# Kernel optimization log

Measured on AMD Instinct MI355X. Metric: run time of the kernel, lower is better.

Reference implementation:

```python
import jax, jax.numpy as jnp
import numpy as np
from jax import lax

B, M = 16384, 128
NUM_LAYERS, OW, OH = 22, 11, 11
MAX_VEC = np.array([9.0, 1.0, 1.0, 10.0, 3.0, 254.0, 1.0, 1.0, 235.0, 8.0, 9.0, 250.0,
                    29.0, 1.0, 1.0, 8.0, 1.0, 1.0, 6.0, 3.0, 1.0, 2.0], dtype=np.float32)


def setup_inputs() -> dict:
    key = jax.random.key(0)
    ks = jax.random.split(key, 20)
    s = 0.05
    return {
        "observations": jax.random.randint(ks[0], (B, M, 3), 0, 255, dtype=jnp.int32),
        "cnn1_w": jax.random.normal(ks[1], (64, 22, 5, 5), jnp.float32) * s,
        "cnn1_b": jnp.zeros((64,), jnp.float32),
        "cnn2_w": jax.random.normal(ks[2], (64, 64, 3, 3), jnp.float32) * s,
        "cnn2_b": jnp.zeros((64,), jnp.float32),
        "fc1_w": jax.random.normal(ks[3], (128, 64), jnp.float32) * s,
        "fc1_b": jnp.zeros((128,), jnp.float32),
        "enc_w": jax.random.normal(ks[4], (128, 128), jnp.float32) * s,
        "enc_b": jnp.zeros((128,), jnp.float32),
        "critic1_w": jax.random.normal(ks[5], (1024, 128), jnp.float32) * s,
        "critic1_b": jnp.zeros((1024,), jnp.float32),
        "value_w": jax.random.normal(ks[6], (1, 1024), jnp.float32) * s,
        "value_b": jnp.zeros((1,), jnp.float32),
        "actor1_w": jax.random.normal(ks[7], (512, 128), jnp.float32) * s,
        "actor1_b": jnp.zeros((512,), jnp.float32),
        "action_emb": jax.random.normal(ks[8], (100, 16), jnp.float32) * s,
        "head0_w": jax.random.normal(ks[9], (9, 528), jnp.float32) * s,
        "head0_b": jnp.zeros((9,), jnp.float32),
        "head1_w": jax.random.normal(ks[10], (10, 528), jnp.float32) * s,
        "head1_b": jnp.zeros((10,), jnp.float32),
    }


def _encode_scatter(observations):
    # zero-out any byte equal to 255 (matches torch in-place masking)
    tok = jnp.where(observations == 255, 0, observations)  # [B, M, 3]
    coords = tok[..., 0].astype(jnp.uint8)
    x = ((coords >> 4) & 15).astype(jnp.int32)
    y = (coords & 15).astype(jnp.int32)
    atr = tok[..., 1].astype(jnp.int32)
    val = tok[..., 2].astype(jnp.float32)
    b, m = atr.shape
    valid = (x < OW) & (y < OH) & (atr < NUM_LAYERS)
    b_idx = jnp.broadcast_to(jnp.arange(b, dtype=jnp.int32)[:, None], (b, m))
    b_idx = jnp.where(valid, b_idx, b)  # route invalid tokens out of bounds -> dropped
    box = jnp.zeros((b, NUM_LAYERS, OW, OH), jnp.float32)
    box = box.at[b_idx, atr, x, y].set(val, mode="drop")
    return box


def _forward(observations, cnn1_w, cnn1_b, cnn2_w, cnn2_b, fc1_w, fc1_b, enc_w, enc_b,
             critic1_w, critic1_b, value_w, value_b, actor1_w, actor1_b, action_emb,
             head0_w, head0_b, head1_w, head1_b):
    box = _encode_scatter(observations)
    x = box / jnp.asarray(MAX_VEC)[None, :, None, None]
    dn = ("NCHW", "OIHW", "NCHW")
    x = lax.conv_general_dilated(x, cnn1_w, (3, 3), "VALID", dimension_numbers=dn) + cnn1_b[None, :, None, None]
    x = lax.conv_general_dilated(x, cnn2_w, (1, 1), "VALID", dimension_numbers=dn) + cnn2_b[None, :, None, None]
    x = x.reshape(x.shape[0], -1)                 # [B, 64]
    x = x @ fc1_w.T + fc1_b                       # [B, 128]
    hidden = x @ enc_w.T + enc_b                  # [B, 128]
    critic = jnp.tanh(hidden @ critic1_w.T + critic1_b)
    value = critic @ value_w.T + value_b          # [B, 1]
    actor = hidden @ actor1_w.T + actor1_b        # [B, 512]
    emb = jnp.broadcast_to(action_emb.mean(axis=0)[None, :], (actor.shape[0], action_emb.shape[1]))
    comb = jnp.concatenate([actor, emb], axis=-1)  # [B, 528]
    logits = jnp.concatenate([comb @ head0_w.T + head0_b, comb @ head1_w.T + head1_b], axis=-1)
    return logits, value


def reference(observations, cnn1_w, cnn1_b, cnn2_w, cnn2_b, fc1_w, fc1_b, enc_w, enc_b,
              critic1_w, critic1_b, value_w, value_b, actor1_w, actor1_b, action_emb,
              head0_w, head0_b, head1_w, head1_b):
    return _forward(observations, cnn1_w, cnn1_b, cnn2_w, cnn2_b, fc1_w, fc1_b, enc_w, enc_b,
                    critic1_w, critic1_b, value_w, value_b, actor1_w, actor1_b, action_emb,
                    head0_w, head0_b, head1_w, head1_b)
```

## Files before the change

kernel.cpp:

```cpp
#include <hip/hip_runtime.h>
#include <math.h>

#define NB 16384
#define NTOK 128
#define NKEY 2662
#define NLOG 19
#define TB 32

typedef __attribute__((ext_vector_type(8))) short short8;
typedef __attribute__((ext_vector_type(4))) float floatx4;

__device__ __constant__ float c_maxv[22] = {
    9.f, 1.f, 1.f, 10.f, 3.f, 254.f, 1.f, 1.f, 235.f, 8.f, 9.f, 250.f,
    29.f, 1.f, 1.f, 8.f, 1.f, 1.f, 6.f, 3.f, 1.f, 2.f};

__device__ __forceinline__ unsigned short f2bf(float f) {
    unsigned u = __float_as_uint(f);
    return (unsigned short)((u + 0x7FFFu + ((u >> 16) & 1u)) >> 16);
}
__device__ __forceinline__ float tanh_fast(float x) {
    float e = __builtin_amdgcn_exp2f(x * 2.885390082f);
    return 1.f - 2.f * __builtin_amdgcn_rcpf(e + 1.f);
}

__global__ __launch_bounds__(256) void k_pre1(
    const float* __restrict__ w1, const float* __restrict__ b1,
    const float* __restrict__ w2, const float* __restrict__ b2,
    const float* __restrict__ fc1w, const float* __restrict__ encw,
    const float* __restrict__ h0w, const float* __restrict__ h1w,
    const float* __restrict__ a1w, const float* __restrict__ aemb,
    const float* __restrict__ c1w,
    float* __restrict__ G, float* __restrict__ E,
    float* __restrict__ h2b, float* __restrict__ emb,
    float* __restrict__ Wlog, unsigned short* __restrict__ c1wb)
{
    __shared__ float s_w2[72 * 65];
    const int bid = blockIdx.x, t = threadIdx.x;
    if (bid < 666) {
        const int v = t & 63;
        const int key_u = __builtin_amdgcn_readfirstlane(bid * 4 + (t >> 6));
        const int key_c = (key_u < NKEY) ? key_u : (NKEY - 1);
        const int c = key_c / 121, rem = key_c % 121, X = rem / 11, Y = rem % 11;

        const int vg0 = t / 72, rg0 = t - vg0 * 72;
        const int base0 = vg0 * 576 + rg0;

        float rw[18];
        {
            int rg = rg0, base = base0;
            #pragma unroll
            for (int r = 0; r < 18; ++r) {
                rw[r] = w2[base];
                rg += 40; base += 1768;
                if (rg >= 72) { rg -= 72; base += 504; }
            }
        }
        float acc = 0.f;
        for (int s = 0; s < 8; ++s) {
            __syncthreads();
            {
                int rg = rg0, vg = vg0;
                #pragma unroll
                for (int r = 0; r < 18; ++r) {
                    s_w2[rg * 65 + vg] = rw[r];
                    rg += 40; vg += 3;
                    if (rg >= 72) { rg -= 72; vg += 1; }
                }
            }
            __syncthreads();
            if (s < 7) {
                int rg = rg0, base = base0 + (s + 1) * 72;
                #pragma unroll
                for (int r = 0; r < 18; ++r) {
                    rw[r] = w2[base];
                    rg += 40; base += 1768;
                    if (rg >= 72) { rg -= 72; base += 504; }
                }
            }
            const int u0 = s * 8;
            #pragma unroll
            for (int ur = 0; ur < 8; ++ur) {
                const int w1base = (u0 + ur) * 550 + c * 25;
                #pragma unroll
                for (int i = 0; i < 3; ++i) {
                    int xi = X - 3 * i;
                    if (xi < 0 || xi > 4) continue;
                    #pragma unroll
                    for (int j = 0; j < 3; ++j) {
                        int yj = Y - 3 * j;
                        if (yj < 0 || yj > 4) continue;
                        acc += s_w2[(ur * 9 + i * 3 + j) * 65 + v] *
                               w1[w1base + xi * 5 + yj];
                    }
                }
            }
        }
        if (key_u < NKEY) G[key_u * 64 + v] = acc;
    } else if (bid < 698) {
        int m = (bid - 666) * 256 + t;
        int h = __builtin_amdgcn_readfirstlane(m >> 6) & 127;
        int v = t & 63;
        float acc = 0.f;
        #pragma unroll 8
        for (int p = 0; p < 128; ++p)
            acc += encw[h * 128 + p] * fc1w[p * 64 + v];
        E[h * 64 + v] = acc;
    } else if (bid == 698) {
        int o = t >> 2, q = t & 3;
        const float* wp = w2 + (o * 64 + q * 16) * 9;
        float s = 0.f;
        #pragma unroll
        for (int ui = 0; ui < 16; ++ui) {
            float ws = 0.f;
            #pragma unroll
            for (int k = 0; k < 9; ++k) ws += wp[ui * 9 + k];
            s += b1[q * 16 + ui] * ws;
        }
        s += __shfl_xor(s, 1, 64);
        s += __shfl_xor(s, 2, 64);
        if (q == 0) h2b[o] = s + b2[o];
    } else if (bid == 699) {
        if (t < 64) {
            int e = t & 15, rq = t >> 4;
            float s = 0.f;
            #pragma unroll
            for (int rr = 0; rr < 25; ++rr) s += aemb[(rq * 25 + rr) * 16 + e];
            s += __shfl_xor(s, 16, 64);
            s += __shfl_xor(s, 32, 64);
            if (t < 16) emb[e] = s * 0.01f;
        }
    } else if (bid < 710) {
        int n = (bid - 700) * 256 + t;
        if (n < NLOG * 128) {
            int o = __builtin_amdgcn_readfirstlane(n >> 7);
            int h = n & 127;
            const float* hw = (o < 9) ? (h0w + o * 528) : (h1w + (o - 9) * 528);
            float acc = 0.f;
            #pragma unroll 8
            for (int a = 0; a < 512; ++a)
                acc += hw[a] * a1w[a * 128 + h];
            Wlog[n] = acc;
        }
    } else {
        int n = (bid - 710) * 256 + t;
        c1wb[n] = f2bf(c1w[n]);
    }
}

__global__ __launch_bounds__(256) void k_pre2(
    const float* __restrict__ G, const float* __restrict__ E,
    const float* __restrict__ h2b, const float* __restrict__ emb,
    const float* __restrict__ fc1w, const float* __restrict__ fc1b,
    const float* __restrict__ encw, const float* __restrict__ encb,
    const float* __restrict__ a1b,
    const float* __restrict__ h0w, const float* __restrict__ h0b,
    const float* __restrict__ h1w, const float* __restrict__ h1b,
    float* __restrict__ Weff, float* __restrict__ beff, float* __restrict__ blog)
{
    __shared__ float s_h2[64];
    __shared__ float s_t[128];
    const int bid = blockIdx.x, t = threadIdx.x;
    if (bid < 1331) {
        int n = bid * 256 + t;
        int key = __builtin_amdgcn_readfirstlane(n >> 7);
        int h = n & 127;
        const float4* E4 = (const float4*)E;
        const float4* G4 = (const float4*)(G + key * 64);
        float acc = 0.f;
        #pragma unroll
        for (int vq = 0; vq < 16; ++vq) {
            float4 e = E4[h * 16 + vq];
            float4 g = G4[vq];
            acc += e.x * g.x + e.y * g.y + e.z * g.z + e.w * g.w;
        }
        Weff[n] = acc / c_maxv[key / 121];
    } else {
        if (t < 64) s_h2[t] = h2b[t];
        __syncthreads();
        if (t < 128) {
            const float4* f4 = (const float4*)(fc1w + t * 64);
            float s = fc1b[t];
            #pragma unroll
            for (int vq = 0; vq < 16; ++vq) {
                float4 w = f4[vq];
                s += w.x * s_h2[vq * 4]     + w.y * s_h2[vq * 4 + 1] +
                     w.z * s_h2[vq * 4 + 2] + w.w * s_h2[vq * 4 + 3];
            }
            s_t[t] = s;
        } else {
            int tp = t - 128;
            int os = tp >> 3, ai = tp & 7;
            #pragma unroll
            for (int rep = 0; rep < 2; ++rep) {
                int o = os + rep * 16;
                int oc = (o < NLOG) ? o : (NLOG - 1);
                const float* hw = (oc < 9) ? (h0w + oc * 528)
                                           : (h1w + (oc - 9) * 528);
                float s = 0.f;
                for (int a = ai; a < 528; a += 8) {
                    float m = (a < 512) ? a1b[a] : emb[a - 512];
                    s += hw[a] * m;
                }
                s += __shfl_xor(s, 1, 64);
                s += __shfl_xor(s, 2, 64);
                s += __shfl_xor(s, 4, 64);
                if (ai == 0 && o < NLOG)
                    blog[o] = s + ((o < 9) ? h0b[o] : h1b[o - 9]);
            }
        }
        __syncthreads();
        if (t < 128) {
            const float4* e4 = (const float4*)(encw + t * 128);
            float s = encb[t];
            #pragma unroll
            for (int pq = 0; pq < 32; ++pq) {
                float4 w = e4[pq];
                s += w.x * s_t[pq * 4]     + w.y * s_t[pq * 4 + 1] +
                     w.z * s_t[pq * 4 + 2] + w.w * s_t[pq * 4 + 3];
            }
            beff[t] = s;
        }
    }
}

__global__ __launch_bounds__(512, 4) void k_main(
    const int* __restrict__ obs,
    const float* __restrict__ Weff, const float* __restrict__ beff,
    const unsigned short* __restrict__ c1wb, const float* __restrict__ c1b,
    const float* __restrict__ vw, const float* __restrict__ vb,
    const float* __restrict__ Wlog, const float* __restrict__ blog,
    float* __restrict__ out)
{
    __shared__ int            s_lst[TB * 32];
    __shared__ float          s_hidden[TB * 128];
    __shared__ unsigned short s_hb[TB * 136];
    __shared__ int            s_cnt[TB];
    __shared__ float          s_val[8 * 32];

    const int tid = threadIdx.x, bid = blockIdx.x;
    const int b0 = bid * TB;

    if (tid < TB) s_cnt[tid] = 0;
    __syncthreads();

    {
        const int gtok0 = b0 * NTOK;
        #pragma unroll
        for (int k = 0; k < TB * NTOK / (512 * 4); ++k) {
            int g = tid + 512 * k;
            const int4* p = (const int4*)(obs + (size_t)(gtok0 + 4 * g) * 3);
            int4 A = p[0], Bv = p[1], Cv = p[2];
            int d[12] = {A.x, A.y, A.z, A.w, Bv.x, Bv.y, Bv.z, Bv.w,
                         Cv.x, Cv.y, Cv.z, Cv.w};
            #pragma unroll
            for (int s = 0; s < 4; ++s) {
                int o0 = d[3 * s], o1 = d[3 * s + 1], o2 = d[3 * s + 2];
                o0 = (o0 == 255) ? 0 : o0;
                o1 = (o1 == 255) ? 0 : o1;
                o2 = (o2 == 255) ? 0 : o2;
                int x = (o0 >> 4) & 15, y = o0 & 15;
                if (x < 11 && y < 11 && o1 < 22) {
                    int tt = 4 * g + s;
                    int bb = tt >> 7, m = tt & 127;
                    int pos = atomicAdd(&s_cnt[bb], 1);
                    if (pos < 32)
                        s_lst[bb * 32 + pos] =
                            (m << 20) | (o2 << 12) | (o1 * 121 + x * 11 + y);
                }
            }
        }
    }
    __syncthreads();

    {
        int bb = tid >> 4, e0 = tid & 15;
        int n = s_cnt[bb]; if (n > 32) n = 32;
        #pragma unroll
        for (int r = 0; r < 2; ++r) {
            int e = e0 + 16 * r;
            if (e < n) {
                int p = s_lst[bb * 32 + e];
                bool dead = false;
                for (int i = 0; i < n; ++i) {
                    int q = s_lst[bb * 32 + i];
                    dead |= (((q ^ p) & 0xFFF) == 0) && (q > p);
                }
                if (dead) s_lst[bb * 32 + e] = p & ~0x000FF000;
            }
        }
    }
    __syncthreads();

    {
        int h = tid & 127, bg = tid >> 7;
        float be = beff[h];
        #pragma unroll
        for (int it = 0; it < 4; ++it) {
            int bbA = bg + it * 8, bbB = bbA + 4;
            int nA = s_cnt[bbA]; if (nA > 32) nA = 32;
            int nB = s_cnt[bbB]; if (nB > 32) nB = 32;
            int nm = (nA > nB) ? nA : nB;
            float aA = be, aB = be;
            for (int i = 0; i < nm; ++i) {
                if (i < nA) {
                    int p = s_lst[bbA * 32 + i];
                    aA += (float)((p >> 12) & 0xFF) * Weff[(p & 0xFFF) * 128 + h];
                }
                if (i < nB) {
                    int p = s_lst[bbB * 32 + i];
                    aB += (float)((p >> 12) & 0xFF) * Weff[(p & 0xFFF) * 128 + h];
                }
            }
            s_hidden[bbA * 128 + h] = aA; s_hb[bbA * 136 + h] = f2bf(aA);
            s_hidden[bbB * 128 + h] = aB; s_hb[bbB * 136 + h] = f2bf(aB);
        }
    }
    __syncthreads();

    {
        const int lane = tid & 63, w = tid >> 6;
        const int lm = lane & 15, quad = lane >> 4;
        short8 af0[4], af1[4];
        #pragma unroll
        for (int kk = 0; kk < 4; ++kk) {
            af0[kk] = *(const short8*)&s_hb[lm * 136 + kk * 32 + quad * 8];
            af1[kk] = *(const short8*)&s_hb[(16 + lm) * 136 + kk * 32 + quad * 8];
        }
        float vp0[4] = {0.f, 0.f, 0.f, 0.f}, vp1[4] = {0.f, 0.f, 0.f, 0.f};
        for (int nt = 0; nt < 8; ++nt) {
            int j = w * 128 + nt * 16 + lm;
            const short8* cp = (const short8*)&c1wb[j * 128];
            floatx4 a0 = {0.f, 0.f, 0.f, 0.f}, a1 = {0.f, 0.f, 0.f, 0.f};
            #pragma unroll
            for (int kk = 0; kk < 4; ++kk) {
                short8 bf = cp[kk * 4 + quad];
                a0 = __builtin_amdgcn_mfma_f32_16x16x32_bf16(af0[kk], bf, a0, 0, 0, 0);
                a1 = __builtin_amdgcn_mfma_f32_16x16x32_bf16(af1[kk], bf, a1, 0, 0, 0);
            }
            float bj = c1b[j], wj = vw[j];
            #pragma unroll
            for (int r = 0; r < 4; ++r) {
                vp0[r] += tanh_fast(a0[r] + bj) * wj;
                vp1[r] += tanh_fast(a1[r] + bj) * wj;
            }
        }
        #pragma unroll
        for (int off = 1; off <= 8; off <<= 1) {
            #pragma unroll
            for (int r = 0; r < 4; ++r) {
                vp0[r] += __shfl_xor(vp0[r], off, 64);
                vp1[r] += __shfl_xor(vp1[r], off, 64);
            }
        }
        if (lm == 0) {
            #pragma unroll
            for (int r = 0; r < 4; ++r) {
                s_val[w * 32 + quad * 4 + r]      = vp0[r];
                s_val[w * 32 + 16 + quad * 4 + r] = vp1[r];
            }
        }
    }
    __syncthreads();
    if (tid < TB) {
        float v = 0.f;
        #pragma unroll
        for (int w = 0; w < 8; ++w) v += s_val[w * 32 + tid];
        out[NB * NLOG + b0 + tid] = v + vb[0];
    }

    {
        const float4* s_h4 = (const float4*)s_hidden;
        const float4* wl4  = (const float4*)Wlog;
        int bl = tid >> 4, oo = tid & 15;
        #pragma unroll
        for (int rep = 0; rep < 2; ++rep) {
            int o = oo + rep * 16;
            if (o < NLOG) {
                float acc = blog[o];
                #pragma unroll
                for (int hq = 0; hq < 32; ++hq) {
                    float4 hv = s_h4[bl * 32 + hq];
                    float4 wl = wl4[o * 32 + hq];
                    acc += wl.x * hv.x + wl.y * hv.y + wl.z * hv.z + wl.w * hv.w;
                }
                out[(b0 + bl) * NLOG + o] = acc;
            }
        }
    }
}

extern "C" void kernel_launch(void* const* d_in, const int* in_sizes, int n_in,
                              void* d_out, int out_size, void* d_ws, size_t ws_size,
                              hipStream_t stream)
{
    const int*   obs  = (const int*)  d_in[0];
    const float* w1   = (const float*)d_in[1];
    const float* b1   = (const float*)d_in[2];
    const float* w2   = (const float*)d_in[3];
    const float* b2   = (const float*)d_in[4];
    const float* fc1w = (const float*)d_in[5];
    const float* fc1b = (const float*)d_in[6];
    const float* encw = (const float*)d_in[7];
    const float* encb = (const float*)d_in[8];
    const float* c1w  = (const float*)d_in[9];
    const float* c1b  = (const float*)d_in[10];
    const float* vw   = (const float*)d_in[11];
    const float* vb   = (const float*)d_in[12];
    const float* a1w  = (const float*)d_in[13];
    const float* a1b  = (const float*)d_in[14];
    const float* aemb = (const float*)d_in[15];
    const float* h0w  = (const float*)d_in[16];
    const float* h0b  = (const float*)d_in[17];
    const float* h1w  = (const float*)d_in[18];
    const float* h1b  = (const float*)d_in[19];

    float* W    = (float*)d_ws;
    float* G    = W;
    float* E    = W + 170368;
    float* h2b  = W + 178560;
    float* emb  = W + 178624;
    float* Weff = W + 178640;
    float* beff = W + 519376;
    float* Wlog = W + 519504;
    float* blog = W + 521936;
    unsigned short* c1wb = (unsigned short*)(W + 524288);

    hipLaunchKernelGGL(k_pre1, dim3(1222), dim3(256), 0, stream,
                       w1, b1, w2, b2, fc1w, encw, h0w, h1w, a1w, aemb, c1w,
                       G, E, h2b, emb, Wlog, c1wb);
    hipLaunchKernelGGL(k_pre2, dim3(1332), dim3(256), 0, stream,
                       G, E, h2b, emb, fc1w, fc1b, encw, encb, a1b,
                       h0w, h0b, h1w, h1b, Weff, beff, blog);
    hipLaunchKernelGGL(k_main, dim3(NB / TB), dim3(512), 0, stream,
                       obs, Weff, beff, c1wb, c1b, vw, vb, Wlog, blog,
                       (float*)d_out);
}
```

Measured before the change: 214.7 us.

## Drop Weff precompute; gather 64-wide G and apply E per tile in main kernel

Removes the second preprocessing kernel that built the 2662x128 effective weight table. The main kernel now gathers from the smaller 64-wide G table into shared memory, then applies the transposed E matrix (staged in LDS) with a small per-tile matmul. The small bias and logit-bias computations are folded into one block of the single preprocessing kernel, and the bf16 weight conversion is vectorised. This saves a launch and halves the gather width, but adds 32KB of LDS plus an extra matmul stage in k_main, which may lower occupancy.

```diff
diff --git a/kernel.cpp b/kernel.cpp
--- a/kernel.cpp
+++ b/kernel.cpp
@@ -23,61 +23,40 @@
     return 1.f - 2.f * __builtin_amdgcn_rcpf(e + 1.f);
 }
 
-__global__ __launch_bounds__(256) void k_pre1(
+__global__ __launch_bounds__(256) void k_pre(
     const float* __restrict__ w1, const float* __restrict__ b1,
     const float* __restrict__ w2, const float* __restrict__ b2,
-    const float* __restrict__ fc1w, const float* __restrict__ encw,
-    const float* __restrict__ h0w, const float* __restrict__ h1w,
-    const float* __restrict__ a1w, const float* __restrict__ aemb,
+    const float* __restrict__ fc1w, const float* __restrict__ fc1b,
+    const float* __restrict__ encw, const float* __restrict__ encb,
+    const float* __restrict__ a1w, const float* __restrict__ a1b,
+    const float* __restrict__ aemb,
+    const float* __restrict__ h0w, const float* __restrict__ h0b,
+    const float* __restrict__ h1w, const float* __restrict__ h1b,
     const float* __restrict__ c1w,
     float* __restrict__ G, float* __restrict__ E,
-    float* __restrict__ h2b, float* __restrict__ emb,
-    float* __restrict__ Wlog, unsigned short* __restrict__ c1wb)
+    float* __restrict__ beff, float* __restrict__ Wlog,
+    float* __restrict__ blog, unsigned short* __restrict__ c1wb)
 {
     __shared__ float s_w2[72 * 65];
+    __shared__ float s_h2[64];
+    __shared__ float s_t[128];
+    __shared__ float s_emb[16];
     const int bid = blockIdx.x, t = threadIdx.x;
     if (bid < 666) {
         const int v = t & 63;
         const int key_u = __builtin_amdgcn_readfirstlane(bid * 4 + (t >> 6));
         const int key_c = (key_u < NKEY) ? key_u : (NKEY - 1);
         const int c = key_c / 121, rem = key_c % 121, X = rem / 11, Y = rem % 11;
-
-        const int vg0 = t / 72, rg0 = t - vg0 * 72;
-        const int base0 = vg0 * 576 + rg0;
-
-        float rw[18];
-        {
-            int rg = rg0, base = base0;
+        float acc = 0.f;
+        for (int u0 = 0; u0 < 64; u0 += 8) {
+            __syncthreads();
             #pragma unroll
             for (int r = 0; r < 18; ++r) {
-                rw[r] = w2[base];
-                rg += 40; base += 1768;
-                if (rg >= 72) { rg -= 72; base += 504; }
-            }
-        }
-        float acc = 0.f;
-        for (int s = 0; s < 8; ++s) {
+                int g = t + 256 * r;
+                int vg = g / 72, rg = g % 72;
+                s_w2[rg * 65 + vg] = w2[vg * 576 + u0 * 9 + rg];
+            }
             __syncthreads();
-            {
-                int rg = rg0, vg = vg0;
-                #pragma unroll
-                for (int r = 0; r < 18; ++r) {
-                    s_w2[rg * 65 + vg] = rw[r];
-                    rg += 40; vg += 3;
-                    if (rg >= 72) { rg -= 72; vg += 1; }
-                }
-            }
-            __syncthreads();
-            if (s < 7) {
-                int rg = rg0, base = base0 + (s + 1) * 72;
-                #pragma unroll
-                for (int r = 0; r < 18; ++r) {
-                    rw[r] = w2[base];
-                    rg += 40; base += 1768;
-                    if (rg >= 72) { rg -= 72; base += 504; }
-                }
-            }
-            const int u0 = s * 8;
             #pragma unroll
             for (int ur = 0; ur < 8; ++ur) {
                 const int w1base = (u0 + ur) * 550 + c * 25;
@@ -95,7 +74,7 @@
                 }
             }
         }
-        if (key_u < NKEY) G[key_u * 64 + v] = acc;
+        if (key_u < NKEY) G[key_u * 64 + v] = acc / c_maxv[c];
     } else if (bid < 698) {
         int m = (bid - 666) * 256 + t;
         int h = __builtin_amdgcn_readfirstlane(m >> 6) & 127;
@@ -104,33 +83,78 @@
         #pragma unroll 8
         for (int p = 0; p < 128; ++p)
             acc += encw[h * 128 + p] * fc1w[p * 64 + v];
-        E[h * 64 + v] = acc;
+        E[v * 128 + h] = acc;
     } else if (bid == 698) {
-        int o = t >> 2, q = t & 3;
-        const float* wp = w2 + (o * 64 + q * 16) * 9;
-        float s = 0.f;
-        #pragma unroll
-        for (int ui = 0; ui < 16; ++ui) {
-            float ws = 0.f;
-            #pragma unroll
-            for (int k = 0; k < 9; ++k) ws += wp[ui * 9 + k];
-            s += b1[q * 16 + ui] * ws;
-        }
-        s += __shfl_xor(s, 1, 64);
-        s += __shfl_xor(s, 2, 64);
-        if (q == 0) h2b[o] = s + b2[o];
-    } else if (bid == 699) {
-        if (t < 64) {
-            int e = t & 15, rq = t >> 4;
+        {
+            int o = t >> 2, q = t & 3;
+            const float* wp = w2 + (o * 64 + q * 16) * 9;
+            float s = 0.f;
+            #pragma unroll
+            for (int ui = 0; ui < 16; ++ui) {
+                float ws = 0.f;
+                #pragma unroll
+                for (int k = 0; k < 9; ++k) ws += wp[ui * 9 + k];
+                s += b1[q * 16 + ui] * ws;
+            }
+            s += __shfl_xor(s, 1, 64);
+            s += __shfl_xor(s, 2, 64);
+            if (q == 0) s_h2[o] = s + b2[o];
+        }
+        __syncthreads();
+        if (t < 128) {
+            const float4* f4 = (const float4*)(fc1w + t * 64);
+            float s = fc1b[t];
+            #pragma unroll
+            for (int vq = 0; vq < 16; ++vq) {
+                float4 w = f4[vq];
+                s += w.x * s_h2[vq * 4]     + w.y * s_h2[vq * 4 + 1] +
+                     w.z * s_h2[vq * 4 + 2] + w.w * s_h2[vq * 4 + 3];
+            }
+            s_t[t] = s;
+        } else if (t < 192) {
+            int lane = t & 63;
+            int e = lane & 15, rq = lane >> 4;
             float s = 0.f;
             #pragma unroll
             for (int rr = 0; rr < 25; ++rr) s += aemb[(rq * 25 + rr) * 16 + e];
             s += __shfl_xor(s, 16, 64);
             s += __shfl_xor(s, 32, 64);
-            if (t < 16) emb[e] = s * 0.01f;
-        }
-    } else if (bid < 710) {
-        int n = (bid - 700) * 256 + t;
+            if (lane < 16) s_emb[e] = s * 0.01f;
+        }
+        __syncthreads();
+        if (t < 128) {
+            const float4* e4 = (const float4*)(encw + t * 128);
+            float s = encb[t];
+            #pragma unroll
+            for (int pq = 0; pq < 32; ++pq) {
+                float4 w = e4[pq];
+                s += w.x * s_t[pq * 4]     + w.y * s_t[pq * 4 + 1] +
+                     w.z * s_t[pq * 4 + 2] + w.w * s_t[pq * 4 + 3];
+            }
+            beff[t] = s;
+        } else {
+            int tp = t - 128;
+            int os = tp >> 3, ai = tp & 7;
+            #pragma unroll
+            for (int rep = 0; rep < 2; ++rep) {
+                int o = os + rep * 16;
+                int oc = (o < NLOG) ? o : (NLOG - 1);
+                const float* hw = (oc < 9) ? (h0w + oc * 528)
+                                           : (h1w + (oc - 9) * 528);
+                float s = 0.f;
+                for (int a = ai; a < 528; a += 8) {
+                    float m = (a < 512) ? a1b[a] : s_emb[a - 512];
+                    s += hw[a] * m;
+                }
+                s += __shfl_xor(s, 1, 64);
+                s += __shfl_xor(s, 2, 64);
+                s += __shfl_xor(s, 4, 64);
+                if (ai == 0 && o < NLOG)
+                    blog[o] = s + ((o < 9) ? h0b[o] : h1b[o - 9]);
+            }
+        }
+    } else if (bid < 709) {
+        int n = (bid - 699) * 256 + t;
         if (n < NLOG * 128) {
             int o = __builtin_amdgcn_readfirstlane(n >> 7);
             int h = n & 127;
@@ -142,90 +166,22 @@
             Wlog[n] = acc;
         }
     } else {
-        int n = (bid - 710) * 256 + t;
-        c1wb[n] = f2bf(c1w[n]);
-    }
-}
-
-__global__ __launch_bounds__(256) void k_pre2(
-    const float* __restrict__ G, const float* __restrict__ E,
-    const float* __restrict__ h2b, const float* __restrict__ emb,
-    const float* __restrict__ fc1w, const float* __restrict__ fc1b,
-    const float* __restrict__ encw, const float* __restrict__ encb,
-    const float* __restrict__ a1b,
-    const float* __restrict__ h0w, const float* __restrict__ h0b,
-    const float* __restrict__ h1w, const float* __restrict__ h1b,
-    float* __restrict__ Weff, float* __restrict__ beff, float* __restrict__ blog)
-{
-    __shared__ float s_h2[64];
-    __shared__ float s_t[128];
-    const int bid = blockIdx.x, t = threadIdx.x;
-    if (bid < 1331) {
-        int n = bid * 256 + t;
-        int key = __builtin_amdgcn_readfirstlane(n >> 7);
-        int h = n & 127;
-        const float4* E4 = (const float4*)E;
-        const float4* G4 = (const float4*)(G + key * 64);
-        float acc = 0.f;
-        #pragma unroll
-        for (int vq = 0; vq < 16; ++vq) {
-            float4 e = E4[h * 16 + vq];
-            float4 g = G4[vq];
-            acc += e.x * g.x + e.y * g.y + e.z * g.z + e.w * g.w;
-        }
-        Weff[n] = acc / c_maxv[key / 121];
-    } else {
-        if (t < 64) s_h2[t] = h2b[t];
-        __syncthreads();
-        if (t < 128) {
-            const float4* f4 = (const float4*)(fc1w + t * 64);
-            float s = fc1b[t];
-            #pragma unroll
-            for (int vq = 0; vq < 16; ++vq) {
-                float4 w = f4[vq];
-                s += w.x * s_h2[vq * 4]     + w.y * s_h2[vq * 4 + 1] +
-                     w.z * s_h2[vq * 4 + 2] + w.w * s_h2[vq * 4 + 3];
-            }
-            s_t[t] = s;
-        } else {
-            int tp = t - 128;
-            int os = tp >> 3, ai = tp & 7;
-            #pragma unroll
-            for (int rep = 0; rep < 2; ++rep) {
-                int o = os + rep * 16;
-                int oc = (o < NLOG) ? o : (NLOG - 1);
-                const float* hw = (oc < 9) ? (h0w + oc * 528)
-                                           : (h1w + (oc - 9) * 528);
-                float s = 0.f;
-                for (int a = ai; a < 528; a += 8) {
-                    float m = (a < 512) ? a1b[a] : emb[a - 512];
-                    s += hw[a] * m;
-                }
-                s += __shfl_xor(s, 1, 64);
-                s += __shfl_xor(s, 2, 64);
-                s += __shfl_xor(s, 4, 64);
-                if (ai == 0 && o < NLOG)
-                    blog[o] = s + ((o < 9) ? h0b[o] : h1b[o - 9]);
-            }
-        }
-        __syncthreads();
-        if (t < 128) {
-            const float4* e4 = (const float4*)(encw + t * 128);
-            float s = encb[t];
-            #pragma unroll
-            for (int pq = 0; pq < 32; ++pq) {
-                float4 w = e4[pq];
-                s += w.x * s_t[pq * 4]     + w.y * s_t[pq * 4 + 1] +
-                     w.z * s_t[pq * 4 + 2] + w.w * s_t[pq * 4 + 3];
-            }
-            beff[t] = s;
-        }
+        int n = ((bid - 709) * 256 + t) * 8;
+        float4 a = *(const float4*)(c1w + n);
+        float4 b4 = *(const float4*)(c1w + n + 4);
+        short8 r;
+        r[0] = (short)f2bf(a.x);  r[1] = (short)f2bf(a.y);
+        r[2] = (short)f2bf(a.z);  r[3] = (short)f2bf(a.w);
+        r[4] = (short)f2bf(b4.x); r[5] = (short)f2bf(b4.y);
+        r[6] = (short)f2bf(b4.z); r[7] = (short)f2bf(b4.w);
+        *(short8*)(c1wb + n) = r;
     }
 }
 
 __global__ __launch_bounds__(512, 4) void k_main(
     const int* __restrict__ obs,
-    const float* __restrict__ Weff, const float* __restrict__ beff,
+    const float* __restrict__ G, const float* __restrict__ E,
+    const float* __restrict__ beff,
     const unsigned short* __restrict__ c1wb, const float* __restrict__ c1b,
     const float* __restrict__ vw, const float* __restrict__ vb,
     const float* __restrict__ Wlog, const float* __restrict__ blog,
@@ -234,11 +190,17 @@
     __shared__ int            s_lst[TB * 32];
     __shared__ float          s_hidden[TB * 128];
     __shared__ unsigned short s_hb[TB * 136];
+    __shared__ float          s_x[TB * 64];
+    __shared__ float          s_E[8192];
     __shared__ int            s_cnt[TB];
     __shared__ float          s_val[8 * 32];
 
     const int tid = threadIdx.x, bid = blockIdx.x;
     const int b0 = bid * TB;
+
+    const float4* E4g = (const float4*)E;
+    float4 e0 = E4g[tid], e1 = E4g[tid + 512],
+           e2 = E4g[tid + 1024], e3 = E4g[tid + 1536];
 
     if (tid < TB) s_cnt[tid] = 0;
     __syncthreads();
@@ -269,15 +231,18 @@
                 }
             }
         }
-    }
-    __syncthreads();
-
-    {
-        int bb = tid >> 4, e0 = tid & 15;
+        float4* sE4 = (float4*)s_E;
+        sE4[tid] = e0; sE4[tid + 512] = e1;
+        sE4[tid + 1024] = e2; sE4[tid + 1536] = e3;
+    }
+    __syncthreads();
+
+    {
+        int bb = tid >> 4, e0i = tid & 15;
         int n = s_cnt[bb]; if (n > 32) n = 32;
         #pragma unroll
         for (int r = 0; r < 2; ++r) {
-            int e = e0 + 16 * r;
+            int e = e0i + 16 * r;
             if (e < n) {
                 int p = s_lst[bb * 32 + e];
                 bool dead = false;
@@ -292,27 +257,54 @@
     __syncthreads();
 
     {
-        int h = tid & 127, bg = tid >> 7;
-        float be = beff[h];
-        #pragma unroll
-        for (int it = 0; it < 4; ++it) {
-            int bbA = bg + it * 8, bbB = bbA + 4;
+        int w = tid >> 6, lane = tid & 63;
+        #pragma unroll
+        for (int jp = 0; jp < 2; ++jp) {
+            int bbA = w * 4 + jp * 2, bbB = bbA + 1;
             int nA = s_cnt[bbA]; if (nA > 32) nA = 32;
             int nB = s_cnt[bbB]; if (nB > 32) nB = 32;
             int nm = (nA > nB) ? nA : nB;
-            float aA = be, aB = be;
+            float aA = 0.f, aB = 0.f;
             for (int i = 0; i < nm; ++i) {
                 if (i < nA) {
                     int p = s_lst[bbA * 32 + i];
-                    aA += (float)((p >> 12) & 0xFF) * Weff[(p & 0xFFF) * 128 + h];
+                    aA += (float)((p >> 12) & 0xFF) * G[(p & 0xFFF) * 64 + lane];
                 }
                 if (i < nB) {
                     int p = s_lst[bbB * 32 + i];
-                    aB += (float)((p >> 12) & 0xFF) * Weff[(p & 0xFFF) * 128 + h];
-                }
-            }
-            s_hidden[bbA * 128 + h] = aA; s_hb[bbA * 136 + h] = f2bf(aA);
-            s_hidden[bbB * 128 + h] = aB; s_hb[bbB * 136 + h] = f2bf(aB);
+                    aB += (float)((p >> 12) & 0xFF) * G[(p & 0xFFF) * 64 + lane];
+                }
+            }
+            s_x[bbA * 64 + lane] = aA;
+            s_x[bbB * 64 + lane] = aB;
+        }
+    }
+    __syncthreads();
+
+    {
+        int g = tid >> 7, h = tid & 127;
+        float be = beff[h];
+        float acc[8];
+        #pragma unroll
+        for (int b = 0; b < 8; ++b) acc[b] = be;
+        const float4* x4 = (const float4*)s_x;
+        #pragma unroll
+        for (int vq = 0; vq < 16; ++vq) {
+            float ev0 = s_E[(vq * 4 + 0) * 128 + h];
+            float ev1 = s_E[(vq * 4 + 1) * 128 + h];
+            float ev2 = s_E[(vq * 4 + 2) * 128 + h];
+            float ev3 = s_E[(vq * 4 + 3) * 128 + h];
+            #pragma unroll
+            for (int b = 0; b < 8; ++b) {
+                float4 xv = x4[(g * 8 + b) * 16 + vq];
+                acc[b] += xv.x * ev0 + xv.y * ev1 + xv.z * ev2 + xv.w * ev3;
+            }
+        }
+        #pragma unroll
+        for (int b = 0; b < 8; ++b) {
+            int bb = g * 8 + b;
+            s_hidden[bb * 128 + h] = acc[b];
+            s_hb[bb * 136 + h] = f2bf(acc[b]);
         }
     }
     __syncthreads();
@@ -359,13 +351,6 @@
                 s_val[w * 32 + 16 + quad * 4 + r] = vp1[r];
             }
         }
-    }
-    __syncthreads();
-    if (tid < TB) {
-        float v = 0.f;
-        #pragma unroll
-        for (int w = 0; w < 8; ++w) v += s_val[w * 32 + tid];
-        out[NB * NLOG + b0 + tid] = v + vb[0];
     }
 
     {
@@ -386,6 +371,13 @@
                 out[(b0 + bl) * NLOG + o] = acc;
             }
         }
+    }
+    __syncthreads();
+    if (tid < TB) {
+        float v = 0.f;
+        #pragma unroll
+        for (int w = 0; w < 8; ++w) v += s_val[w * 32 + tid];
+        out[NB * NLOG + b0 + tid] = v + vb[0];
     }
 }
 
@@ -417,21 +409,16 @@
     float* W    = (float*)d_ws;
     float* G    = W;
     float* E    = W + 170368;
-    float* h2b  = W + 178560;
-    float* emb  = W + 178624;
-    float* Weff = W + 178640;
-    float* beff = W + 519376;
-    float* Wlog = W + 519504;
-    float* blog = W + 521936;
-    unsigned short* c1wb = (unsigned short*)(W + 524288);
-
-    hipLaunchKernelGGL(k_pre1, dim3(1222), dim3(256), 0, stream,
-                       w1, b1, w2, b2, fc1w, encw, h0w, h1w, a1w, aemb, c1w,
-                       G, E, h2b, emb, Wlog, c1wb);
-    hipLaunchKernelGGL(k_pre2, dim3(1332), dim3(256), 0, stream,
-                       G, E, h2b, emb, fc1w, fc1b, encw, encb, a1b,
-                       h0w, h0b, h1w, h1b, Weff, beff, blog);
+    float* beff = W + 178560;
+    float* Wlog = W + 178688;
+    float* blog = W + 181120;
+    unsigned short* c1wb = (unsigned short*)(W + 181152);
+
+    hipLaunchKernelGGL(k_pre, dim3(773), dim3(256), 0, stream,
+                       w1, b1, w2, b2, fc1w, fc1b, encw, encb, a1w, a1b, aemb,
+                       h0w, h0b, h1w, h1b, c1w,
+                       G, E, beff, Wlog, blog, c1wb);
     hipLaunchKernelGGL(k_main, dim3(NB / TB), dim3(512), 0, stream,
-                       obs, Weff, beff, c1wb, c1b, vw, vb, Wlog, blog,
+                       obs, G, E, beff, c1wb, c1b, vw, vb, Wlog, blog,
                        (float*)d_out);
 }
```

Result: faster. 188.8 us (median of 2 runs) (-12.1%).
